# Optimization experiments

Measured on AMD Instinct MI355X. Metric: run time of the kernel, lower is better.

Reference implementation:

```python
import jax, jax.numpy as jnp
import numpy as np

B, S, D, H = 4, 2048, 1024, 16
DH = D // H


def setup_inputs() -> dict:
    key = jax.random.key(0)
    k1, k2, k3, k4, k5 = jax.random.split(key, 5)
    X = jax.random.normal(k1, (B, S, D), dtype=jnp.float32)
    W1 = jax.random.normal(k2, (3 * D, D), dtype=jnp.float32) * 0.02
    b1 = jax.random.normal(k3, (3 * D,), dtype=jnp.float32) * 0.01
    W2 = jax.random.normal(k4, (D, D), dtype=jnp.float32) * 0.02
    b2 = jax.random.normal(k5, (D,), dtype=jnp.float32) * 0.01
    return {"X": X, "W1": W1, "b1": b1, "W2": W2, "b2": b2}


def reference(X, W1, b1, W2, b2):
    b, s, d = X.shape
    # fused QKV projection (nn.Linear: y = x @ W.T + b)
    Y = X @ W1.T + b1                                   # [B,S,3D]
    Q, K, V = jnp.split(Y, 3, axis=2)                   # each [B,S,D]
    # reshape(x): view (B,S,H,DH) then permute(0,2,3,1) -> [B,H,DH,S]
    q = Q.reshape(b, s, H, DH).transpose(0, 2, 3, 1)    # [B,H,DH,S]
    v = V.reshape(b, s, H, DH).transpose(0, 2, 3, 1)    # [B,H,DH,S]
    # reshape(x, k=True): permute(0,2,1,3) -> [B,H,S,DH]
    k = K.reshape(b, s, H, DH).transpose(0, 2, 1, 3)    # [B,H,S,DH]
    # w = q @ k / sqrt(q.size(-1)) ; note q.size(-1) == S in this layout
    w = jnp.einsum('bhds,bhse->bhde', q, k) / jnp.sqrt(jnp.asarray(s, X.dtype))  # [B,H,DH,DH]
    w = jax.nn.softmax(w, axis=-1)
    out = jnp.einsum('bhde,bhes->bhds', w, v)           # [B,H,DH,S]
    # cat(): raw contiguous view of [B,H,DH,S] into [B,S,H*DH] (memory-order reshape)
    out = out.reshape(b, s, H * DH)                     # [B,S,D]
    return out @ W2.T + b2
```

## Files before the change

kernel.cpp:

```cpp
#include <hip/hip_runtime.h>
#include <stdint.h>

#define B_ 4
#define S_ 2048
#define D_ 1024
#define H_ 16
#define DH_ 64
#define M_TOT (B_*S_)
#define N1_ (3*D_)
#define K_ D_
#define NCH 8

typedef __bf16 bf16_8 __attribute__((ext_vector_type(8)));
typedef float  f32x4  __attribute__((ext_vector_type(4)));
typedef unsigned short u16;

typedef __attribute__((address_space(1))) const void* gas_t;
typedef __attribute__((address_space(3))) void*       las_t;

__device__ __forceinline__ unsigned short f2bf(float f) {
    union { float f; unsigned u; } v; v.f = f;
    unsigned r = v.u + 0x7FFFu + ((v.u >> 16) & 1u);
    return (unsigned short)(r >> 16);
}

__device__ __forceinline__ void async_ld16(const void* g, void* l) {
    __builtin_amdgcn_global_load_lds((gas_t)g, (las_t)l, 16, 0, 0);
}

__global__ __launch_bounds__(256)
void cast_kernel(const float* __restrict__ X, const float* __restrict__ W1,
                 const float* __restrict__ W2, unsigned short* __restrict__ Xb,
                 unsigned short* __restrict__ W1b, unsigned short* __restrict__ W2b) {
    const int nX  = (M_TOT * K_) / 4;
    const int nW1 = (N1_ * K_) / 4;
    int i = blockIdx.x * 256 + threadIdx.x;
    const float4* src; unsigned short* dst; int j;
    if (i < nX)            { src = (const float4*)X;  dst = Xb;  j = i; }
    else if (i < nX + nW1) { src = (const float4*)W1; dst = W1b; j = i - nX; }
    else                   { src = (const float4*)W2; dst = W2b; j = i - nX - nW1; }
    float4 v = src[j];
    ushort4 o;
    o.x = f2bf(v.x); o.y = f2bf(v.y); o.z = f2bf(v.z); o.w = f2bf(v.w);
    ((ushort4*)dst)[j] = o;
}

template<int N, int NBX, int EPI>
__global__ __launch_bounds__(256)
void gemm_bt(const unsigned short* __restrict__ A,
             const unsigned short* __restrict__ Bm,
             const float* __restrict__ bias,
             void* __restrict__ C, int K,
             u16* __restrict__ QT, u16* __restrict__ KT, u16* __restrict__ Vh) {
    __shared__ unsigned short As[128 * 64];
    __shared__ unsigned short Bs[128 * 64];
    const int t    = threadIdx.x;
    const int wid  = t >> 6;
    const int lane = t & 63;
    const int lrow = lane & 15;
    const int lq   = lane >> 4;

    const int lid  = blockIdx.y * NBX + blockIdx.x;
    const int xcd  = lid & 7;
    const int slot = lid >> 3;
    const int by   = xcd * (gridDim.y >> 3) + slot / NBX;
    const int bx   = slot % NBX;
    const int m0   = by * 128;
    const int n0   = bx * 128;

    const int wm   = (wid >> 1) * 64;
    const int wn   = (wid & 1) * 64;

    f32x4 acc[4][4] = {};

    for (int k0 = 0; k0 < K; k0 += 64) {
#pragma unroll
        for (int p = 0; p < 4; p++) {
            const int c   = p * 256 + t;
            const int row = c >> 3;
            const int kb  = (c & 7) ^ (row & 7);
            async_ld16(A  + (size_t)(m0 + row) * K + k0 + kb * 8, (char*)As + c * 16);
            async_ld16(Bm + (size_t)(n0 + row) * K + k0 + kb * 8, (char*)Bs + c * 16);
        }
        __syncthreads();

#pragma unroll
        for (int ks = 0; ks < 2; ks++) {
            bf16_8 af[4], bfr[4];
#pragma unroll
            for (int mt = 0; mt < 4; mt++) {
                const int r  = wm + mt * 16 + lrow;
                const int kb = (ks * 4 + lq) ^ (r & 7);
                af[mt] = *(const bf16_8*)(As + (r * 8 + kb) * 8);
            }
#pragma unroll
            for (int nt = 0; nt < 4; nt++) {
                const int r  = wn + nt * 16 + lrow;
                const int kb = (ks * 4 + lq) ^ (r & 7);
                bfr[nt] = *(const bf16_8*)(Bs + (r * 8 + kb) * 8);
            }
#pragma unroll
            for (int mt = 0; mt < 4; mt++)
#pragma unroll
                for (int nt = 0; nt < 4; nt++)
                    acc[mt][nt] = __builtin_amdgcn_mfma_f32_16x16x32_bf16(af[mt], bfr[nt], acc[mt][nt], 0, 0, 0);
        }
        __syncthreads();
    }

#pragma unroll
    for (int nt = 0; nt < 4; nt++) {
        const int col = n0 + wn + nt * 16 + lrow;
        const float bv = bias[col];
#pragma unroll
        for (int mt = 0; mt < 4; mt++) {
            const int row = m0 + wm + mt * 16 + lq * 4;
            f32x4 a = acc[mt][nt];
            if constexpr (EPI == 2) {
                ushort4 o;
                o.x = f2bf(a[0] + bv); o.y = f2bf(a[1] + bv);
                o.z = f2bf(a[2] + bv); o.w = f2bf(a[3] + bv);
                const int b = row >> 11, s = row & 2047;
                const int d = col & 63;
                if (col < 1024) {
                    *(ushort4*)(QT + ((size_t)(b * 16 + (col >> 6)) * 64 + d) * (size_t)S_ + s) = o;
                } else if (col < 2048) {
                    *(ushort4*)(KT + ((size_t)(b * 16 + ((col >> 6) - 16)) * 64 + d) * (size_t)S_ + s) = o;
                } else {
                    const int h = (col >> 6) - 32, e = col & 63;
                    u16* vp = Vh + ((size_t)(b * 16 + h) * S_ + s) * 64 + e;
                    vp[0]   = o.x;
                    vp[64]  = o.y;
                    vp[128] = o.z;
                    vp[192] = o.w;
                }
            } else {
                float* Cp = (float*)C;
#pragma unroll
                for (int i = 0; i < 4; i++)
                    Cp[(size_t)(row + i) * N + col] = a[i] + bv;
            }
        }
    }
}

__global__ __launch_bounds__(256)
void attn_qk(const u16* __restrict__ QT, const u16* __restrict__ KT,
             float* __restrict__ Scp) {
    __shared__ u16 Qs[64 * 64];
    __shared__ u16 Ks[64 * 64];
    const int bh = blockIdx.x, ch = blockIdx.y;
    const int t = threadIdx.x, wid = t >> 6, lane = t & 63;
    const int lrow = lane & 15, lq = lane >> 4;
    const int wm2 = (wid >> 1) * 32, wn2 = (wid & 1) * 32;
    const u16* Qh = QT + (size_t)bh * 64 * S_;
    const u16* Kh = KT + (size_t)bh * 64 * S_;

    f32x4 acc[2][2] = {};
    for (int kt = 0; kt < 4; kt++) {
        const int s0 = ch * 256 + kt * 64;
#pragma unroll
        for (int p = 0; p < 4; p++) {
            const int c   = p * 256 + t;
            const int cc  = c & 511;
            const int row = cc >> 3;
            const int kb  = (cc & 7) ^ (row & 7);
            if (p < 2)
                async_ld16(Qh + (size_t)row * S_ + s0 + kb * 8, (char*)Qs + cc * 16);
            else
                async_ld16(Kh + (size_t)row * S_ + s0 + kb * 8, (char*)Ks + cc * 16);
        }
        __syncthreads();
#pragma unroll
        for (int ks = 0; ks < 2; ks++) {
            bf16_8 aq[2], bk[2];
#pragma unroll
            for (int mt = 0; mt < 2; mt++) {
                const int r  = wm2 + mt * 16 + lrow;
                const int kb = (ks * 4 + lq) ^ (r & 7);
                aq[mt] = *(const bf16_8*)(Qs + (r * 8 + kb) * 8);
            }
#pragma unroll
            for (int nt = 0; nt < 2; nt++) {
                const int r  = wn2 + nt * 16 + lrow;
                const int kb = (ks * 4 + lq) ^ (r & 7);
                bk[nt] = *(const bf16_8*)(Ks + (r * 8 + kb) * 8);
            }
#pragma unroll
            for (int mt = 0; mt < 2; mt++)
#pragma unroll
                for (int nt = 0; nt < 2; nt++)
                    acc[mt][nt] = __builtin_amdgcn_mfma_f32_16x16x32_bf16(aq[mt], bk[nt], acc[mt][nt], 0, 0, 0);
        }
        __syncthreads();
    }

    float* out = Scp + (size_t)(bh * NCH + ch) * 4096;
#pragma unroll
    for (int mt = 0; mt < 2; mt++)
#pragma unroll
        for (int nt = 0; nt < 2; nt++)
#pragma unroll
            for (int i = 0; i < 4; i++)
                out[(wm2 + mt * 16 + lq * 4 + i) * 64 + wn2 + nt * 16 + lrow] = acc[mt][nt][i];
}

__global__ __launch_bounds__(256)
void attn_softmax(const float* __restrict__ Scp, unsigned short* __restrict__ Wb) {
    const int bh = blockIdx.x;
    const int t = threadIdx.x;
    const int d = t >> 2, q = t & 3;
    float s[16] = {};
#pragma unroll
    for (int c = 0; c < NCH; c++) {
        const float4* p = (const float4*)(Scp + ((size_t)(bh * NCH + c) * 64 + d) * 64 + q * 16);
#pragma unroll
        for (int j = 0; j < 4; j++) {
            float4 v = p[j];
            s[j*4+0] += v.x; s[j*4+1] += v.y; s[j*4+2] += v.z; s[j*4+3] += v.w;
        }
    }
    const float scale = 0.022097086912079608f;
    float m = -3.0e38f;
#pragma unroll
    for (int i = 0; i < 16; i++) { s[i] *= scale; m = fmaxf(m, s[i]); }
    m = fmaxf(m, __shfl_xor(m, 1));
    m = fmaxf(m, __shfl_xor(m, 2));
    float sum = 0.f;
#pragma unroll
    for (int i = 0; i < 16; i++) { s[i] = __expf(s[i] - m); sum += s[i]; }
    sum += __shfl_xor(sum, 1);
    sum += __shfl_xor(sum, 2);
    const float inv = 1.0f / sum;
    unsigned short* w = Wb + (size_t)bh * 4096 + d * 64 + q * 16;
    ushort4 o0, o1, o2, o3;
    o0.x=f2bf(s[0]*inv);  o0.y=f2bf(s[1]*inv);  o0.z=f2bf(s[2]*inv);  o0.w=f2bf(s[3]*inv);
    o1.x=f2bf(s[4]*inv);  o1.y=f2bf(s[5]*inv);  o1.z=f2bf(s[6]*inv);  o1.w=f2bf(s[7]*inv);
    o2.x=f2bf(s[8]*inv);  o2.y=f2bf(s[9]*inv);  o2.z=f2bf(s[10]*inv); o2.w=f2bf(s[11]*inv);
    o3.x=f2bf(s[12]*inv); o3.y=f2bf(s[13]*inv); o3.z=f2bf(s[14]*inv); o3.w=f2bf(s[15]*inv);
    ((ushort4*)w)[0]=o0; ((ushort4*)w)[1]=o1; ((ushort4*)w)[2]=o2; ((ushort4*)w)[3]=o3;
}

__global__ __launch_bounds__(256)
void attn_pv(const u16* __restrict__ Wb, const u16* __restrict__ Vh,
             u16* __restrict__ O) {
    __shared__ u16 Ws[64 * 64];
    __shared__ u16 Vs[256 * 64];
    const int bh = blockIdx.x, sc = blockIdx.y;
    const int t = threadIdx.x, wid = t >> 6, lane = t & 63;
    const int lrow = lane & 15, lq = lane >> 4;
    const u16* Wh = Wb + (size_t)bh * 4096;
    const u16* Vp = Vh + ((size_t)bh * S_ + sc * 256) * 64;

#pragma unroll
    for (int j = 0; j < 2; j++) {
        const int c = j * 256 + t;
        const int row = c >> 3, kb = (c & 7) ^ (row & 7);
        async_ld16(Wh + row * 64 + kb * 8, (char*)Ws + c * 16);
    }
#pragma unroll
    for (int p = 0; p < 8; p++) {
        const int c = p * 256 + t;
        const int row = c >> 3, kb = (c & 7) ^ (row & 7);
        async_ld16(Vp + (size_t)row * 64 + kb * 8, (char*)Vs + c * 16);
    }
    __syncthreads();

    f32x4 acc[4][4] = {};
#pragma unroll
    for (int ks = 0; ks < 2; ks++) {
        bf16_8 af[4], bfr[4];
#pragma unroll
        for (int mt = 0; mt < 4; mt++) {
            const int r  = mt * 16 + lrow;
            const int kb = (ks * 4 + lq) ^ (r & 7);
            af[mt] = *(const bf16_8*)(Ws + (r * 8 + kb) * 8);
        }
#pragma unroll
        for (int nt = 0; nt < 4; nt++) {
            const int r  = wid * 64 + nt * 16 + lrow;
            const int kb = (ks * 4 + lq) ^ (r & 7);
            bfr[nt] = *(const bf16_8*)(Vs + (r * 8 + kb) * 8);
        }
#pragma unroll
        for (int mt = 0; mt < 4; mt++)
#pragma unroll
            for (int nt = 0; nt < 4; nt++)
                acc[mt][nt] = __builtin_amdgcn_mfma_f32_16x16x32_bf16(af[mt], bfr[nt], acc[mt][nt], 0, 0, 0);
    }

    const size_t obase = (size_t)bh * (DH_ * S_);
    const int s0 = sc * 256 + wid * 64;
#pragma unroll
    for (int mt = 0; mt < 4; mt++)
#pragma unroll
        for (int nt = 0; nt < 4; nt++) {
            const int d = mt * 16 + lq * 4;
            const int s = s0 + nt * 16 + lrow;
#pragma unroll
            for (int i = 0; i < 4; i++)
                O[obase + (size_t)(d + i) * S_ + s] = f2bf(acc[mt][nt][i]);
        }
}

extern "C" void kernel_launch(void* const* d_in, const int* in_sizes, int n_in,
                              void* d_out, int out_size, void* d_ws, size_t ws_size,
                              hipStream_t stream) {
    const float* X  = (const float*)d_in[0];
    const float* W1 = (const float*)d_in[1];
    const float* b1 = (const float*)d_in[2];
    const float* W2 = (const float*)d_in[3];
    const float* b2 = (const float*)d_in[4];

    char* ws = (char*)d_ws;
    unsigned short* Xb  = (unsigned short*)(ws + 0);
    unsigned short* W1b = (unsigned short*)(ws + (16u << 20));
    unsigned short* W2b = (unsigned short*)(ws + (22u << 20));
    unsigned short* QT  = (unsigned short*)(ws + (24u << 20));
    unsigned short* KT  = (unsigned short*)(ws + (40u << 20));
    unsigned short* Vh  = (unsigned short*)(ws + (56u << 20));
    unsigned short* Wb  = (unsigned short*)(ws + 0);
    unsigned short* Ob  = (unsigned short*)(ws + (1u << 20));
    float* Scp = (float*)d_out;

    cast_kernel<<<12288, 256, 0, stream>>>(X, W1, W2, Xb, W1b, W2b);
    gemm_bt<N1_, N1_/128, 2><<<dim3(N1_ / 128, M_TOT / 128), 256, 0, stream>>>(
        Xb, W1b, b1, nullptr, K_, QT, KT, Vh);
    attn_qk<<<dim3(64, NCH), 256, 0, stream>>>(QT, KT, Scp);
    attn_softmax<<<64, 256, 0, stream>>>(Scp, Wb);
    attn_pv<<<dim3(64, NCH), 256, 0, stream>>>(Wb, Vh, Ob);
    gemm_bt<D_, D_/128, 0><<<dim3(D_ / 128, M_TOT / 128), 256, 0, stream>>>(
        Ob, W2b, b2, d_out, K_, nullptr, nullptr, nullptr);
}
```

Baseline: 204.0 us.

## Split QK reduction into more chunks and parallelize softmax across rows

The split-K count for the Q·K^T reduction rises from 8 to 32 chunks, so each attn_qk block now loads a single 64-wide tile and there are 2048 blocks instead of 512. The softmax kernel is spread over four row segments per head, with 16 threads per row doing four columns each, which gives 256 blocks instead of 64. attn_pv keeps its own grid of 8. The aim is better occupancy in these two small kernels, at the price of four times more fp32 partial-sum traffic for softmax to read and more reduction work.

Result: slower. 216.7 us (+6.2%).

```diff
diff --git a/kernel.cpp b/kernel.cpp
--- a/kernel.cpp
+++ b/kernel.cpp
@@ -9,7 +9,7 @@
 #define M_TOT (B_*S_)
 #define N1_ (3*D_)
 #define K_ D_
-#define NCH 8
+#define NCH 32
 
 typedef __bf16 bf16_8 __attribute__((ext_vector_type(8)));
 typedef float  f32x4  __attribute__((ext_vector_type(4)));
@@ -155,44 +155,42 @@
     const int wm2 = (wid >> 1) * 32, wn2 = (wid & 1) * 32;
     const u16* Qh = QT + (size_t)bh * 64 * S_;
     const u16* Kh = KT + (size_t)bh * 64 * S_;
+    const int s0 = ch * 64;
+
+#pragma unroll
+    for (int p = 0; p < 4; p++) {
+        const int c   = p * 256 + t;
+        const int cc  = c & 511;
+        const int row = cc >> 3;
+        const int kb  = (cc & 7) ^ (row & 7);
+        if (p < 2)
+            async_ld16(Qh + (size_t)row * S_ + s0 + kb * 8, (char*)Qs + cc * 16);
+        else
+            async_ld16(Kh + (size_t)row * S_ + s0 + kb * 8, (char*)Ks + cc * 16);
+    }
+    __syncthreads();
 
     f32x4 acc[2][2] = {};
-    for (int kt = 0; kt < 4; kt++) {
-        const int s0 = ch * 256 + kt * 64;
-#pragma unroll
-        for (int p = 0; p < 4; p++) {
-            const int c   = p * 256 + t;
-            const int cc  = c & 511;
-            const int row = cc >> 3;
-            const int kb  = (cc & 7) ^ (row & 7);
-            if (p < 2)
-                async_ld16(Qh + (size_t)row * S_ + s0 + kb * 8, (char*)Qs + cc * 16);
-            else
-                async_ld16(Kh + (size_t)row * S_ + s0 + kb * 8, (char*)Ks + cc * 16);
-        }
-        __syncthreads();
-#pragma unroll
-        for (int ks = 0; ks < 2; ks++) {
-            bf16_8 aq[2], bk[2];
-#pragma unroll
-            for (int mt = 0; mt < 2; mt++) {
-                const int r  = wm2 + mt * 16 + lrow;
-                const int kb = (ks * 4 + lq) ^ (r & 7);
-                aq[mt] = *(const bf16_8*)(Qs + (r * 8 + kb) * 8);
-            }
-#pragma unroll
-            for (int nt = 0; nt < 2; nt++) {
-                const int r  = wn2 + nt * 16 + lrow;
-                const int kb = (ks * 4 + lq) ^ (r & 7);
-                bk[nt] = *(const bf16_8*)(Ks + (r * 8 + kb) * 8);
-            }
-#pragma unroll
-            for (int mt = 0; mt < 2; mt++)
-#pragma unroll
-                for (int nt = 0; nt < 2; nt++)
-                    acc[mt][nt] = __builtin_amdgcn_mfma_f32_16x16x32_bf16(aq[mt], bk[nt], acc[mt][nt], 0, 0, 0);
-        }
-        __syncthreads();
+#pragma unroll
+    for (int ks = 0; ks < 2; ks++) {
+        bf16_8 aq[2], bk[2];
+#pragma unroll
+        for (int mt = 0; mt < 2; mt++) {
+            const int r  = wm2 + mt * 16 + lrow;
+            const int kb = (ks * 4 + lq) ^ (r & 7);
+            aq[mt] = *(const bf16_8*)(Qs + (r * 8 + kb) * 8);
+        }
+#pragma unroll
+        for (int nt = 0; nt < 2; nt++) {
+            const int r  = wn2 + nt * 16 + lrow;
+            const int kb = (ks * 4 + lq) ^ (r & 7);
+            bk[nt] = *(const bf16_8*)(Ks + (r * 8 + kb) * 8);
+        }
+#pragma unroll
+        for (int mt = 0; mt < 2; mt++)
+#pragma unroll
+            for (int nt = 0; nt < 2; nt++)
+                acc[mt][nt] = __builtin_amdgcn_mfma_f32_16x16x32_bf16(aq[mt], bk[nt], acc[mt][nt], 0, 0, 0);
     }
 
     float* out = Scp + (size_t)(bh * NCH + ch) * 4096;
@@ -207,38 +205,35 @@
 
 __global__ __launch_bounds__(256)
 void attn_softmax(const float* __restrict__ Scp, unsigned short* __restrict__ Wb) {
-    const int bh = blockIdx.x;
+    const int bh = blockIdx.x, seg = blockIdx.y;
     const int t = threadIdx.x;
-    const int d = t >> 2, q = t & 3;
-    float s[16] = {};
+    const int d = seg * 16 + (t >> 4), q = t & 15;
+    float s[4] = {};
 #pragma unroll
     for (int c = 0; c < NCH; c++) {
-        const float4* p = (const float4*)(Scp + ((size_t)(bh * NCH + c) * 64 + d) * 64 + q * 16);
-#pragma unroll
-        for (int j = 0; j < 4; j++) {
-            float4 v = p[j];
-            s[j*4+0] += v.x; s[j*4+1] += v.y; s[j*4+2] += v.z; s[j*4+3] += v.w;
-        }
+        float4 v = *(const float4*)(Scp + ((size_t)(bh * NCH + c) * 64 + d) * 64 + q * 4);
+        s[0] += v.x; s[1] += v.y; s[2] += v.z; s[3] += v.w;
     }
     const float scale = 0.022097086912079608f;
     float m = -3.0e38f;
 #pragma unroll
-    for (int i = 0; i < 16; i++) { s[i] *= scale; m = fmaxf(m, s[i]); }
+    for (int i = 0; i < 4; i++) { s[i] *= scale; m = fmaxf(m, s[i]); }
     m = fmaxf(m, __shfl_xor(m, 1));
     m = fmaxf(m, __shfl_xor(m, 2));
+    m = fmaxf(m, __shfl_xor(m, 4));
+    m = fmaxf(m, __shfl_xor(m, 8));
     float sum = 0.f;
 #pragma unroll
-    for (int i = 0; i < 16; i++) { s[i] = __expf(s[i] - m); sum += s[i]; }
+    for (int i = 0; i < 4; i++) { s[i] = __expf(s[i] - m); sum += s[i]; }
     sum += __shfl_xor(sum, 1);
     sum += __shfl_xor(sum, 2);
+    sum += __shfl_xor(sum, 4);
+    sum += __shfl_xor(sum, 8);
     const float inv = 1.0f / sum;
-    unsigned short* w = Wb + (size_t)bh * 4096 + d * 64 + q * 16;
-    ushort4 o0, o1, o2, o3;
-    o0.x=f2bf(s[0]*inv);  o0.y=f2bf(s[1]*inv);  o0.z=f2bf(s[2]*inv);  o0.w=f2bf(s[3]*inv);
-    o1.x=f2bf(s[4]*inv);  o1.y=f2bf(s[5]*inv);  o1.z=f2bf(s[6]*inv);  o1.w=f2bf(s[7]*inv);
-    o2.x=f2bf(s[8]*inv);  o2.y=f2bf(s[9]*inv);  o2.z=f2bf(s[10]*inv); o2.w=f2bf(s[11]*inv);
-    o3.x=f2bf(s[12]*inv); o3.y=f2bf(s[13]*inv); o3.z=f2bf(s[14]*inv); o3.w=f2bf(s[15]*inv);
-    ((ushort4*)w)[0]=o0; ((ushort4*)w)[1]=o1; ((ushort4*)w)[2]=o2; ((ushort4*)w)[3]=o3;
+    ushort4 o;
+    o.x = f2bf(s[0] * inv); o.y = f2bf(s[1] * inv);
+    o.z = f2bf(s[2] * inv); o.w = f2bf(s[3] * inv);
+    *(ushort4*)(Wb + (size_t)bh * 4096 + d * 64 + q * 4) = o;
 }
 
 __global__ __launch_bounds__(256)
@@ -327,8 +322,8 @@
     gemm_bt<N1_, N1_/128, 2><<<dim3(N1_ / 128, M_TOT / 128), 256, 0, stream>>>(
         Xb, W1b, b1, nullptr, K_, QT, KT, Vh);
     attn_qk<<<dim3(64, NCH), 256, 0, stream>>>(QT, KT, Scp);
-    attn_softmax<<<64, 256, 0, stream>>>(Scp, Wb);
-    attn_pv<<<dim3(64, NCH), 256, 0, stream>>>(Wb, Vh, Ob);
+    attn_softmax<<<dim3(64, 4), 256, 0, stream>>>(Scp, Wb);
+    attn_pv<<<dim3(64, 8), 256, 0, stream>>>(Wb, Vh, Ob);
     gemm_bt<D_, D_/128, 0><<<dim3(D_ / 128, M_TOT / 128), 256, 0, stream>>>(
         Ob, W2b, b2, d_out, K_, nullptr, nullptr, nullptr);
 }
```
